# Performance work log

Hardware: AMD Instinct MI355X
Metric: run time of the kernel (lower is better)

The kernel has to match this reference:

```python
import jax, jax.numpy as jnp
import numpy as np

B, T, N, C = 2, 8, 10242, 64
K, NBR, O = 9, 7, 64


def setup_inputs() -> dict:
    key = jax.random.key(0)
    k1, k2, k3, k4, k5 = jax.random.split(key, 5)
    x = jax.random.normal(k1, (B, T, N, C), dtype=jnp.float32)
    index = jax.random.randint(k2, (N, NBR), 0, N, dtype=jnp.int64)
    itp_mat = jax.random.uniform(k3, (N, NBR, K), dtype=jnp.float32)
    conv_w = jax.random.normal(k4, (O, C, 1, K), dtype=jnp.float32) * (1.0 / np.sqrt(C * K))
    conv_b = jax.random.normal(k5, (O,), dtype=jnp.float32) * 0.01
    return {"x": x, "index": index, "itp_mat": itp_mat, "conv_w": conv_w, "conv_b": conv_b}


def reference(x, index, itp_mat, conv_w, conv_b):
    b, t, n, c = x.shape
    o = conv_w.shape[0]
    # (B,T,N,C) -> (B*T, C, N)
    feats = x.reshape(b * t, n, c).transpose(0, 2, 1)
    # gather neighbors: (BT, C, N, NBR)
    nb = feats[:, :, index]
    # per-node interpolation matmul: (BT, C, N, K)
    itp = jnp.einsum('bcnj,njk->bcnk', nb, itp_mat)
    # Conv2d with kernel (1,K) on width K collapses K fully: (BT, O, N)
    out = jnp.einsum('bcnk,ock->bon', itp, conv_w[:, :, 0, :]) + conv_b[None, :, None]
    # (B, T, O, N) -> (B, T, N, O)
    return out.reshape(b, t, o, n).transpose(0, 1, 3, 2)
```

## Files before the change

kernel.cpp:

```cpp
#include <hip/hip_runtime.h>

#define BT    16
#define NN    10242
#define CC    64
#define KK    9
#define NBR_  7
#define OO    64
#define CK    576
#define MT    16
#define RS    584
#define KT    18

using frag  = __attribute__((ext_vector_type(8))) short;
using f32x4 = __attribute__((ext_vector_type(4))) float;

static __device__ __forceinline__ unsigned short f2bf(float f) {
    union { float f; unsigned u; } v; v.f = f;
    unsigned r = v.u + 0x7fffu + ((v.u >> 16) & 1u);
    return (unsigned short)(r >> 16);
}

__global__ void pack_w_kernel(const float* __restrict__ w, unsigned short* __restrict__ wb) {
    int i = blockIdx.x * blockDim.x + threadIdx.x;
    if (i >= KT * 4 * 64 * 8) return;
    int j  = i & 7;
    int l  = (i >> 3) & 63;
    int ct = (i >> 9) & 3;
    int t  = i >> 11;
    int q  = t * 32 + (l >> 4) * 8 + j;
    int o  = ct * 16 + (l & 15);
    int c, k;
    if (q < 512) { c = (q & 255) >> 2; k = (q >> 8) * 4 + (q & 3); }
    else         { c = q - 512;        k = 8; }
    wb[i] = f2bf(w[(o * CC + c) * KK + k]);
}

__global__ __launch_bounds__(256, 6) void sphere_conv_kernel(
    const float* __restrict__ x,
    const int*   __restrict__ index,
    const float* __restrict__ m,
    const unsigned short* __restrict__ wb,
    const float* __restrict__ bias,
    float*       __restrict__ out)
{
    __shared__ unsigned short itp_s[MT * RS];

    const int tid  = threadIdx.x;
    const int bt   = blockIdx.x;
    const int n0   = blockIdx.y * MT;
    const int w    = tid >> 6;
    const int lane = tid & 63;

    {
        const float* xbt = x + (size_t)bt * NN * CC;
        #pragma unroll
        for (int r = 0; r < 4; ++r) {
            const int ns = w * 4 + r;
            int n  = n0 + ns;
            int nu = __builtin_amdgcn_readfirstlane(n < NN ? n : (NN - 1));
            const int*   ip = index + nu * NBR_;
            const float* mp = m + nu * (NBR_ * KK);
            float xv[NBR_];
            #pragma unroll
            for (int j = 0; j < NBR_; ++j) {
                const int idj = ip[j];
                xv[j] = xbt[(size_t)idj * CC + lane];
            }
            float acc[KK];
            #pragma unroll
            for (int k = 0; k < KK; ++k) acc[k] = 0.f;
            #pragma unroll
            for (int j = 0; j < NBR_; ++j)
                #pragma unroll
                for (int k = 0; k < KK; ++k)
                    acc[k] = fmaf(xv[j], mp[j * KK + k], acc[k]);

            unsigned short h[KK];
            #pragma unroll
            for (int k = 0; k < KK; ++k) h[k] = f2bf(acc[k]);
            uint2 q0, q1;
            q0.x = (unsigned)h[0] | ((unsigned)h[1] << 16);
            q0.y = (unsigned)h[2] | ((unsigned)h[3] << 16);
            q1.x = (unsigned)h[4] | ((unsigned)h[5] << 16);
            q1.y = (unsigned)h[6] | ((unsigned)h[7] << 16);
            unsigned short* row = &itp_s[ns * RS];
            *(uint2*)(&row[lane * 4])       = q0;
            *(uint2*)(&row[256 + lane * 4]) = q1;
            row[512 + lane] = h[8];
        }
    }
    __syncthreads();

    const int ct   = w;
    const int am   = lane & 15;
    const int half = lane >> 4;

    f32x4 acc = (f32x4){0.f, 0.f, 0.f, 0.f};

    const unsigned short* arow = &itp_s[am * RS + half * 8];
    const frag* wbf = (const frag*)wb;

    #pragma unroll
    for (int t = 0; t < KT; ++t) {
        const frag a = *(const frag*)(arow + t * 32);
        const frag b = wbf[(t * 4 + ct) * 64 + lane];
        acc = __builtin_amdgcn_mfma_f32_16x16x32_bf16(a, b, acc, 0, 0, 0);
    }

    const size_t obase = (size_t)bt * NN * OO;
    {
        const int o  = ct * 16 + am;
        const float bo = bias[o];
        #pragma unroll
        for (int i = 0; i < 4; ++i) {
            const int n = n0 + half * 4 + i;
            if (n < NN) out[obase + (size_t)n * OO + o] = acc[i] + bo;
        }
    }
}

extern "C" void kernel_launch(void* const* d_in, const int* in_sizes, int n_in,
                              void* d_out, int out_size, void* d_ws, size_t ws_size,
                              hipStream_t stream) {
    const float* x      = (const float*)d_in[0];
    const int*   index  = (const int*)  d_in[1];
    const float* m      = (const float*)d_in[2];
    const float* conv_w = (const float*)d_in[3];
    const float* conv_b = (const float*)d_in[4];
    float* out = (float*)d_out;
    unsigned short* wb = (unsigned short*)d_ws;

    {
        const int total = KT * 4 * 64 * 8;
        pack_w_kernel<<<(total + 255) / 256, 256, 0, stream>>>(conv_w, wb);
    }
    {
        dim3 grid(BT, (NN + MT - 1) / MT);
        sphere_conv_kernel<<<grid, 256, 0, stream>>>(x, index, m, wb, conv_b, out);
    }
}
```

Baseline: 148.3 us.

## Process four batch-time slices per block, reusing index and interpolation loads

Each block now handles four (b,t) slices instead of one. Within a block the slices are taken in pairs: one pass loads index and itp_mat once, gathers x for two slices, and runs the interpolation FMAs on two-wide vectors. The second slice's bf16 results wait in registers until the first slice's MFMA finishes, then go to LDS for a second MFMA. This cuts redundant index/matrix loads and weight fragment reloads, at the cost of four times fewer blocks, more registers, and extra barriers that serialise gather and MFMA phases.

```diff
diff --git a/kernel.cpp b/kernel.cpp
--- a/kernel.cpp
+++ b/kernel.cpp
@@ -6,13 +6,14 @@
 #define KK    9
 #define NBR_  7
 #define OO    64
-#define CK    576
 #define MT    16
 #define RS    584
 #define KT    18
+#define BG    4
 
 using frag  = __attribute__((ext_vector_type(8))) short;
 using f32x4 = __attribute__((ext_vector_type(4))) float;
+using f32x2 = __attribute__((ext_vector_type(2))) float;
 
 static __device__ __forceinline__ unsigned short f2bf(float f) {
     union { float f; unsigned u; } v; v.f = f;
@@ -46,76 +47,117 @@
     __shared__ unsigned short itp_s[MT * RS];
 
     const int tid  = threadIdx.x;
-    const int bt   = blockIdx.x;
+    const int btg  = blockIdx.x;
     const int n0   = blockIdx.y * MT;
     const int w    = tid >> 6;
     const int lane = tid & 63;
 
-    {
-        const float* xbt = x + (size_t)bt * NN * CC;
+    const int ct   = w;
+    const int am   = lane & 15;
+    const int half = lane >> 4;
+    const unsigned short* arow = &itp_s[am * RS + half * 8];
+    const frag* wbf = (const frag*)wb;
+    const float bo = bias[ct * 16 + am];
+
+    #pragma unroll
+    for (int ip = 0; ip < BG / 2; ++ip) {
+        const int bt0 = btg * BG + ip * 2;
+        const float* xb0 = x + (size_t)bt0 * NN * CC;
+
+        uint2 sq0[4], sq1[4];
+        unsigned short sh8[4];
+
         #pragma unroll
         for (int r = 0; r < 4; ++r) {
             const int ns = w * 4 + r;
             int n  = n0 + ns;
             int nu = __builtin_amdgcn_readfirstlane(n < NN ? n : (NN - 1));
-            const int*   ip = index + nu * NBR_;
-            const float* mp = m + nu * (NBR_ * KK);
-            float xv[NBR_];
+            const int*   idp = index + nu * NBR_;
+            const float* mp  = m + nu * (NBR_ * KK);
+            f32x2 xv[NBR_];
             #pragma unroll
             for (int j = 0; j < NBR_; ++j) {
-                const int idj = ip[j];
-                xv[j] = xbt[(size_t)idj * CC + lane];
+                const int idj = idp[j];
+                const float* p = xb0 + (size_t)idj * CC + lane;
+                xv[j][0] = p[0];
+                xv[j][1] = p[NN * CC];
             }
-            float acc[KK];
+            f32x2 acc[KK];
             #pragma unroll
-            for (int k = 0; k < KK; ++k) acc[k] = 0.f;
+            for (int k = 0; k < KK; ++k) acc[k] = (f32x2){0.f, 0.f};
             #pragma unroll
-            for (int j = 0; j < NBR_; ++j)
+            for (int j = 0; j < NBR_; ++j) {
                 #pragma unroll
-                for (int k = 0; k < KK; ++k)
-                    acc[k] = fmaf(xv[j], mp[j * KK + k], acc[k]);
-
-            unsigned short h[KK];
+                for (int k = 0; k < KK; ++k) {
+                    const float mjk = mp[j * KK + k];
+                    acc[k] = __builtin_elementwise_fma(xv[j], (f32x2){mjk, mjk}, acc[k]);
+                }
+            }
+            unsigned short h0[KK], h1[KK];
             #pragma unroll
-            for (int k = 0; k < KK; ++k) h[k] = f2bf(acc[k]);
+            for (int k = 0; k < KK; ++k) { h0[k] = f2bf(acc[k][0]); h1[k] = f2bf(acc[k][1]); }
             uint2 q0, q1;
-            q0.x = (unsigned)h[0] | ((unsigned)h[1] << 16);
-            q0.y = (unsigned)h[2] | ((unsigned)h[3] << 16);
-            q1.x = (unsigned)h[4] | ((unsigned)h[5] << 16);
-            q1.y = (unsigned)h[6] | ((unsigned)h[7] << 16);
+            q0.x = (unsigned)h0[0] | ((unsigned)h0[1] << 16);
+            q0.y = (unsigned)h0[2] | ((unsigned)h0[3] << 16);
+            q1.x = (unsigned)h0[4] | ((unsigned)h0[5] << 16);
+            q1.y = (unsigned)h0[6] | ((unsigned)h0[7] << 16);
             unsigned short* row = &itp_s[ns * RS];
             *(uint2*)(&row[lane * 4])       = q0;
             *(uint2*)(&row[256 + lane * 4]) = q1;
-            row[512 + lane] = h[8];
+            row[512 + lane] = h0[8];
+            sq0[r].x = (unsigned)h1[0] | ((unsigned)h1[1] << 16);
+            sq0[r].y = (unsigned)h1[2] | ((unsigned)h1[3] << 16);
+            sq1[r].x = (unsigned)h1[4] | ((unsigned)h1[5] << 16);
+            sq1[r].y = (unsigned)h1[6] | ((unsigned)h1[7] << 16);
+            sh8[r]   = h1[8];
         }
-    }
-    __syncthreads();
+        __syncthreads();
 
-    const int ct   = w;
-    const int am   = lane & 15;
-    const int half = lane >> 4;
+        {
+            f32x4 acc = (f32x4){0.f, 0.f, 0.f, 0.f};
+            #pragma unroll
+            for (int t = 0; t < KT; ++t) {
+                const frag a = *(const frag*)(arow + t * 32);
+                const frag b = wbf[(t * 4 + ct) * 64 + lane];
+                acc = __builtin_amdgcn_mfma_f32_16x16x32_bf16(a, b, acc, 0, 0, 0);
+            }
+            const size_t obase = (size_t)bt0 * NN * OO;
+            const int o = ct * 16 + am;
+            #pragma unroll
+            for (int i = 0; i < 4; ++i) {
+                const int n = n0 + half * 4 + i;
+                if (n < NN) out[obase + (size_t)n * OO + o] = acc[i] + bo;
+            }
+        }
+        __syncthreads();
 
-    f32x4 acc = (f32x4){0.f, 0.f, 0.f, 0.f};
+        #pragma unroll
+        for (int r = 0; r < 4; ++r) {
+            const int ns = w * 4 + r;
+            unsigned short* row = &itp_s[ns * RS];
+            *(uint2*)(&row[lane * 4])       = sq0[r];
+            *(uint2*)(&row[256 + lane * 4]) = sq1[r];
+            row[512 + lane] = sh8[r];
+        }
+        __syncthreads();
 
-    const unsigned short* arow = &itp_s[am * RS + half * 8];
-    const frag* wbf = (const frag*)wb;
-
-    #pragma unroll
-    for (int t = 0; t < KT; ++t) {
-        const frag a = *(const frag*)(arow + t * 32);
-        const frag b = wbf[(t * 4 + ct) * 64 + lane];
-        acc = __builtin_amdgcn_mfma_f32_16x16x32_bf16(a, b, acc, 0, 0, 0);
-    }
-
-    const size_t obase = (size_t)bt * NN * OO;
-    {
-        const int o  = ct * 16 + am;
-        const float bo = bias[o];
-        #pragma unroll
-        for (int i = 0; i < 4; ++i) {
-            const int n = n0 + half * 4 + i;
-            if (n < NN) out[obase + (size_t)n * OO + o] = acc[i] + bo;
+        {
+            f32x4 acc = (f32x4){0.f, 0.f, 0.f, 0.f};
+            #pragma unroll
+            for (int t = 0; t < KT; ++t) {
+                const frag a = *(const frag*)(arow + t * 32);
+                const frag b = wbf[(t * 4 + ct) * 64 + lane];
+                acc = __builtin_amdgcn_mfma_f32_16x16x32_bf16(a, b, acc, 0, 0, 0);
+            }
+            const size_t obase = (size_t)(bt0 + 1) * NN * OO;
+            const int o = ct * 16 + am;
+            #pragma unroll
+            for (int i = 0; i < 4; ++i) {
+                const int n = n0 + half * 4 + i;
+                if (n < NN) out[obase + (size_t)n * OO + o] = acc[i] + bo;
+            }
         }
+        __syncthreads();
     }
 }
 
@@ -135,7 +177,7 @@
         pack_w_kernel<<<(total + 255) / 256, 256, 0, stream>>>(conv_w, wb);
     }
     {
-        dim3 grid(BT, (NN + MT - 1) / MT);
+        dim3 grid(BT / BG, (NN + MT - 1) / MT);
         sphere_conv_kernel<<<grid, 256, 0, stream>>>(x, index, m, wb, conv_b, out);
     }
 }
```

Measured after the change: 324.4 us. +118.8%, slower.

## Process two batch slices per block with packed FMA and split MFMA accumulators

Applied to the files above, without the earlier changes.

Each block now handles two bt slices in a loop, so the index and interpolation-matrix rows and the weight fragments are reused across slices, and the grid shrinks to half as many blocks. The gather loads for all four rows are issued before the compute, packed f32x2 FMAs replace scalar FMAs for the interpolation step, and the MFMA chain is split into two independent accumulators to shorten the dependency chain. It adds an extra __syncthreads per iteration and serializes two slices within a block, which lowers parallelism and may raise register pressure.

```diff
diff --git a/kernel.cpp b/kernel.cpp
--- a/kernel.cpp
+++ b/kernel.cpp
@@ -6,13 +6,14 @@
 #define KK    9
 #define NBR_  7
 #define OO    64
-#define CK    576
 #define MT    16
 #define RS    584
 #define KT    18
+#define BG    2
 
 using frag  = __attribute__((ext_vector_type(8))) short;
 using f32x4 = __attribute__((ext_vector_type(4))) float;
+using f32x2 = __attribute__((ext_vector_type(2))) float;
 
 static __device__ __forceinline__ unsigned short f2bf(float f) {
     union { float f; unsigned u; } v; v.f = f;
@@ -46,76 +47,87 @@
     __shared__ unsigned short itp_s[MT * RS];
 
     const int tid  = threadIdx.x;
-    const int bt   = blockIdx.x;
+    const int btg  = blockIdx.x;
     const int n0   = blockIdx.y * MT;
     const int w    = tid >> 6;
     const int lane = tid & 63;
 
-    {
+    const int ct   = w;
+    const int am   = lane & 15;
+    const int half = lane >> 4;
+    const unsigned short* arow = &itp_s[am * RS + half * 8];
+    const frag* wbf = (const frag*)wb;
+    const float bo = bias[ct * 16 + am];
+
+    #pragma unroll
+    for (int ib = 0; ib < BG; ++ib) {
+        const int bt = btg * BG + ib;
         const float* xbt = x + (size_t)bt * NN * CC;
+
+        float xv[4][NBR_];
+        const float* mrow[4];
         #pragma unroll
         for (int r = 0; r < 4; ++r) {
             const int ns = w * 4 + r;
             int n  = n0 + ns;
             int nu = __builtin_amdgcn_readfirstlane(n < NN ? n : (NN - 1));
-            const int*   ip = index + nu * NBR_;
-            const float* mp = m + nu * (NBR_ * KK);
-            float xv[NBR_];
+            const int* idp = index + nu * NBR_;
+            mrow[r] = m + nu * (NBR_ * KK);
+            #pragma unroll
+            for (int j = 0; j < NBR_; ++j)
+                xv[r][j] = xbt[(size_t)idp[j] * CC + lane];
+        }
+
+        #pragma unroll
+        for (int r = 0; r < 4; ++r) {
+            const int ns = w * 4 + r;
+            const float* mp = mrow[r];
+            f32x2 a01 = {0.f, 0.f}, a23 = {0.f, 0.f};
+            f32x2 a45 = {0.f, 0.f}, a67 = {0.f, 0.f};
+            float a8 = 0.f;
             #pragma unroll
             for (int j = 0; j < NBR_; ++j) {
-                const int idj = ip[j];
-                xv[j] = xbt[(size_t)idj * CC + lane];
+                const float xj = xv[r][j];
+                const f32x2 xx = {xj, xj};
+                a01 = __builtin_elementwise_fma(xx, (f32x2){mp[j*KK+0], mp[j*KK+1]}, a01);
+                a23 = __builtin_elementwise_fma(xx, (f32x2){mp[j*KK+2], mp[j*KK+3]}, a23);
+                a45 = __builtin_elementwise_fma(xx, (f32x2){mp[j*KK+4], mp[j*KK+5]}, a45);
+                a67 = __builtin_elementwise_fma(xx, (f32x2){mp[j*KK+6], mp[j*KK+7]}, a67);
+                a8  = fmaf(xj, mp[j*KK+8], a8);
             }
-            float acc[KK];
-            #pragma unroll
-            for (int k = 0; k < KK; ++k) acc[k] = 0.f;
-            #pragma unroll
-            for (int j = 0; j < NBR_; ++j)
-                #pragma unroll
-                for (int k = 0; k < KK; ++k)
-                    acc[k] = fmaf(xv[j], mp[j * KK + k], acc[k]);
-
-            unsigned short h[KK];
-            #pragma unroll
-            for (int k = 0; k < KK; ++k) h[k] = f2bf(acc[k]);
             uint2 q0, q1;
-            q0.x = (unsigned)h[0] | ((unsigned)h[1] << 16);
-            q0.y = (unsigned)h[2] | ((unsigned)h[3] << 16);
-            q1.x = (unsigned)h[4] | ((unsigned)h[5] << 16);
-            q1.y = (unsigned)h[6] | ((unsigned)h[7] << 16);
+            q0.x = (unsigned)f2bf(a01[0]) | ((unsigned)f2bf(a01[1]) << 16);
+            q0.y = (unsigned)f2bf(a23[0]) | ((unsigned)f2bf(a23[1]) << 16);
+            q1.x = (unsigned)f2bf(a45[0]) | ((unsigned)f2bf(a45[1]) << 16);
+            q1.y = (unsigned)f2bf(a67[0]) | ((unsigned)f2bf(a67[1]) << 16);
             unsigned short* row = &itp_s[ns * RS];
             *(uint2*)(&row[lane * 4])       = q0;
             *(uint2*)(&row[256 + lane * 4]) = q1;
-            row[512 + lane] = h[8];
+            row[512 + lane] = f2bf(a8);
         }
-    }
-    __syncthreads();
+        __syncthreads();
 
-    const int ct   = w;
-    const int am   = lane & 15;
-    const int half = lane >> 4;
-
-    f32x4 acc = (f32x4){0.f, 0.f, 0.f, 0.f};
-
-    const unsigned short* arow = &itp_s[am * RS + half * 8];
-    const frag* wbf = (const frag*)wb;
-
-    #pragma unroll
-    for (int t = 0; t < KT; ++t) {
-        const frag a = *(const frag*)(arow + t * 32);
-        const frag b = wbf[(t * 4 + ct) * 64 + lane];
-        acc = __builtin_amdgcn_mfma_f32_16x16x32_bf16(a, b, acc, 0, 0, 0);
-    }
-
-    const size_t obase = (size_t)bt * NN * OO;
-    {
-        const int o  = ct * 16 + am;
-        const float bo = bias[o];
-        #pragma unroll
-        for (int i = 0; i < 4; ++i) {
-            const int n = n0 + half * 4 + i;
-            if (n < NN) out[obase + (size_t)n * OO + o] = acc[i] + bo;
+        {
+            f32x4 aa = (f32x4){0.f, 0.f, 0.f, 0.f};
+            f32x4 ab = (f32x4){0.f, 0.f, 0.f, 0.f};
+            #pragma unroll
+            for (int t = 0; t < KT; t += 2) {
+                const frag a0 = *(const frag*)(arow + t * 32);
+                const frag b0 = wbf[(t * 4 + ct) * 64 + lane];
+                aa = __builtin_amdgcn_mfma_f32_16x16x32_bf16(a0, b0, aa, 0, 0, 0);
+                const frag a1 = *(const frag*)(arow + (t + 1) * 32);
+                const frag b1 = wbf[((t + 1) * 4 + ct) * 64 + lane];
+                ab = __builtin_amdgcn_mfma_f32_16x16x32_bf16(a1, b1, ab, 0, 0, 0);
+            }
+            const size_t obase = (size_t)bt * NN * OO;
+            const int o = ct * 16 + am;
+            #pragma unroll
+            for (int i = 0; i < 4; ++i) {
+                const int n = n0 + half * 4 + i;
+                if (n < NN) out[obase + (size_t)n * OO + o] = aa[i] + ab[i] + bo;
+            }
         }
+        __syncthreads();
     }
 }
 
@@ -135,7 +147,7 @@
         pack_w_kernel<<<(total + 255) / 256, 256, 0, stream>>>(conv_w, wb);
     }
     {
-        dim3 grid(BT, (NN + MT - 1) / MT);
+        dim3 grid(BT / BG, (NN + MT - 1) / MT);
         sphere_conv_kernel<<<grid, 256, 0, stream>>>(x, index, m, wb, conv_b, out);
     }
 }
```

Result: no change. 149.0 us (+0.5%).
